# Performance work log

Measured on AMD Instinct MI355X. Metric: run time of the kernel, lower is better.

The kernel has to match this reference:

```python
import jax, jax.numpy as jnp
import numpy as np

DIM = 512
HEADS = 4
HEAD_DIM = DIM // HEADS
SCALE = HEAD_DIM ** -0.5


def _lin(x, W, b):
    # torch nn.Linear: y = x @ W.T + b, W is [out, in]
    return jnp.einsum('...i,oi->...o', x, W) + b


def setup_inputs() -> dict:
    key = jax.random.key(0)
    ks = jax.random.split(key, 20)
    f1 = jax.random.normal(ks[0], (4, 5, DIM, 10, 10), dtype=jnp.float32)
    f2 = jax.random.normal(ks[1], (4, 75, DIM, 10, 10), dtype=jnp.float32)
    names = ['k1', 'v1', 'q2', 'k2', 'v2', 'o1', 'o2']
    inp = {'f1': f1, 'f2': f2}
    for i, nm in enumerate(names):
        inp['W' + nm] = 0.02 * jax.random.normal(ks[2 + 2 * i], (DIM, DIM), dtype=jnp.float32)
        inp['b' + nm] = 0.02 * jax.random.normal(ks[3 + 2 * i], (DIM,), dtype=jnp.float32)
    return inp


def _forward(f1, f2, Wk1, bk1, Wv1, bv1, Wq2, bq2, Wk2, bk2, Wv2, bv2, Wo1, bo1, Wo2, bo2):
    B, n1, C, H, W = f1.shape
    n2 = f2.shape[1]
    L = H * W
    # [B,n,C,H,W] -> [B,n,L,C]
    f1t = f1.reshape(B, n1, C, L).transpose(0, 1, 3, 2)
    f2t = f2.reshape(B, n2, C, L).transpose(0, 1, 3, 2)

    def split_heads(x, n):  # [B,n,L,C] -> [B,heads,n*L,hd]
        return x.reshape(B, n * L, HEADS, HEAD_DIM).transpose(0, 2, 1, 3)

    def merge_heads(x, n):  # [B,heads,n*L,hd] -> [B,n,L,C]
        return x.transpose(0, 2, 1, 3).reshape(B, n, L, C)

    K1 = split_heads(_lin(f1t, Wk1, bk1), n1)
    V1 = split_heads(_lin(f1t, Wv1, bv1), n1)
    Q2 = split_heads(_lin(f2t, Wq2, bq2), n2)
    K2 = split_heads(_lin(f2t, Wk2, bk2), n2)  # computed as in original, unused downstream
    V2 = split_heads(_lin(f2t, Wv2, bv2), n2)

    # Query attends to support: [B,h,n2*L,n1*L]
    att_q = jax.nn.softmax(jnp.einsum('bhqd,bhkd->bhqk', Q2, K1) * SCALE, axis=-1)
    out2 = jnp.einsum('bhqk,bhkd->bhqd', att_q, V1)
    out2 = _lin(merge_heads(out2, n2), Wo2, bo2)
    out2 = out2.transpose(0, 1, 3, 2).reshape(B, n2, C, H, W)

    # Support attends to query: [B,h,n1*L,n2*L]
    att_s = jax.nn.softmax(jnp.einsum('bhsd,bhqd->bhsq', K1, Q2) * SCALE, axis=-1)
    out1 = jnp.einsum('bhsq,bhqd->bhsd', att_s, V2)
    out1 = _lin(merge_heads(out1, n1), Wo1, bo1)
    out1 = out1.transpose(0, 1, 3, 2).reshape(B, n1, C, H, W)
    return (out1, out2)


def reference(f1, f2, Wk1, bk1, Wv1, bv1, Wq2, bq2, Wk2, bk2, Wv2, bv2, Wo1, bo1, Wo2, bo2):
    return _forward(f1, f2, Wk1, bk1, Wv1, bv1, Wq2, bq2, Wk2, bk2, Wv2, bv2, Wo1, bo1, Wo2, bo2)
```

## Files before the change

kernel.cpp:

```cpp
#include <hip/hip_runtime.h>
#include <hip/hip_bf16.h>


#define QSCL  (0.08838834764831845f * 1.4426950408889634f)
#define KSPL  8
#define NRB2  59
#define NRB1  4

using bf16x8 = __attribute__((ext_vector_type(8))) short;
using f32x4  = __attribute__((ext_vector_type(4))) float;

__device__ inline ushort f2bf(float x) {
    union { float f; unsigned u; } v; v.f = x;
    unsigned r = v.u + 0x7fff + ((v.u >> 16) & 1);
    return (ushort)(r >> 16);
}

__device__ inline void gll16(const ushort* g, ushort* l) {
    __builtin_amdgcn_global_load_lds(
        (const __attribute__((address_space(1))) void*)g,
        (__attribute__((address_space(3))) void*)l, 16, 0, 0);
}

struct PreArgs { const float* w[6]; float s[6]; const float* f1; const float* f2; };

__global__ __launch_bounds__(256) void pre_kernel(
    PreArgs pa, ushort* __restrict__ Wb,
    ushort* __restrict__ f1t, ushort* __restrict__ f2t)
{
    __shared__ ushort Ts[100 * 136];
    const int t   = threadIdx.x;
    const int bid = blockIdx.x;

    if (bid < 1536) {
        const int wsel = bid >> 8;
        const float* src = pa.w[wsel];
        const float sc = pa.s[wsel];
        ushort* d = Wb + (size_t)wsel * 262144;
        const int idx = ((bid & 255) * 256 + t) * 4;
        const float4 v = *(const float4*)(src + idx);
        ushort4 o;
        o.x = f2bf(v.x * sc); o.y = f2bf(v.y * sc);
        o.z = f2bf(v.z * sc); o.w = f2bf(v.w * sc);
        *(ushort4*)(d + idx) = o;
        return;
    }

    const int bn = bid - 1536;
    const float* Xb;
    ushort* Yb;
    if (bn < 20) { Xb = pa.f1 + (size_t)bn * 51200;        Yb = f1t + (size_t)bn * 51200; }
    else         { Xb = pa.f2 + (size_t)(bn - 20) * 51200; Yb = f2t + (size_t)(bn - 20) * 51200; }

    for (int c0 = 0; c0 < 512; c0 += 128) {
        __syncthreads();
        #pragma unroll
        for (int i = 0; i < 50; ++i) {
            const int id = i * 256 + t;
            const int c = id / 100, l = id - c * 100;
            Ts[l * 136 + c] = f2bf(Xb[(size_t)(c0 + c) * 100 + l]);
        }
        __syncthreads();
        #pragma unroll
        for (int i = 0; i < 7; ++i) {
            const int id = i * 256 + t;
            if (id < 1600) {
                const int cg = id & 15, l = id >> 4;
                *(uint4*)(Yb + (size_t)l * 512 + c0 + cg * 8) =
                    *(const uint4*)&Ts[l * 136 + cg * 8];
            }
        }
    }
}

struct GemmJob {
    const ushort* A; const ushort* B;
    const float* bias; void* C;
    size_t sA, sB, sC;
    float bscale;
    int ldC, Mrows, Ncols, gx, gy, fastn, baxis, nblk;
};

struct GemmJobs { GemmJob j0, j1, j2, j3; int ntot; };

template<int EPI>
__global__ __launch_bounds__(256) void gemm_nt(GemmJobs J)
{
    __shared__ ushort smem[17408];
    ushort* As = smem;
    ushort* Bs = smem + 8192;

    const int ntot = J.ntot;
    const int q8 = ntot >> 3, r8 = ntot & 7;
    const int xcd = blockIdx.x & 7, ii = blockIdx.x >> 3;
    const int work = (xcd < r8 ? xcd * (q8 + 1)
                               : r8 * (q8 + 1) + (xcd - r8) * q8) + ii;

    GemmJob j; int id;
    {
        const int c0 = J.j0.nblk;
        const int c1 = c0 + J.j1.nblk;
        const int c2 = c1 + J.j2.nblk;
        if (work < c0)      { j = J.j0; id = work; }
        else if (work < c1) { j = J.j1; id = work - c0; }
        else if (work < c2) { j = J.j2; id = work - c1; }
        else                { j = J.j3; id = work - c2; }
    }

    const int fx = id % j.gx;
    const int rem = id / j.gx;
    const int fy = rem % j.gy;
    const int bz = rem / j.gy;
    const int m0 = (j.fastn ? fy : fx) * 128;
    const int n0 = (j.fastn ? fx : fy) * 128;

    const int t    = threadIdx.x;
    const int lane = t & 63;
    const int w    = t >> 6;
    const int mw   = (w >> 1) * 64;
    const int nw   = (w & 1) * 64;
    const int Mrows = j.Mrows, Ncols = j.Ncols, ldC = j.ldC;
    const ushort* Ab = j.A + (size_t)bz * j.sA;
    const ushort* Bb = j.B + (size_t)bz * j.sB;
    const float* bias = j.bias;

    f32x4 acc[4][4];
    #pragma unroll
    for (int i = 0; i < 4; ++i)
        #pragma unroll
        for (int jj = 0; jj < 4; ++jj) acc[i][jj] = (f32x4){0.f, 0.f, 0.f, 0.f};

    const int lr = lane >> 3;
    const int cb = lane & 7;

    for (int k0 = 0; k0 < 512; k0 += 64) {
        if (k0) __syncthreads();
        #pragma unroll
        for (int i = 0; i < 4; ++i) {
            const int row = w * 32 + i * 8 + lr;
            const int ar = min(m0 + row, Mrows - 1);
            gll16(Ab + (size_t)ar * 512 + k0 + ((cb ^ (row & 7)) * 8),
                  As + (w * 32 + i * 8) * 64);
            const int br = min(n0 + row, Ncols - 1);
            gll16(Bb + (size_t)br * 512 + k0 + ((cb ^ (row & 7)) * 8),
                  Bs + (w * 32 + i * 8) * 64);
        }
        __syncthreads();
        #pragma unroll
        for (int ks = 0; ks < 2; ++ks) {
            bf16x8 af[4], bv[4];
            #pragma unroll
            for (int mf = 0; mf < 4; ++mf) {
                const int row = mw + mf * 16 + (lane & 15);
                af[mf] = *(const bf16x8*)((const char*)As + row * 128 +
                          ((ks * 64 + (lane >> 4) * 16) ^ ((row & 7) << 4)));
            }
            #pragma unroll
            for (int nf = 0; nf < 4; ++nf) {
                const int row = nw + nf * 16 + (lane & 15);
                bv[nf] = *(const bf16x8*)((const char*)Bs + row * 128 +
                          ((ks * 64 + (lane >> 4) * 16) ^ ((row & 7) << 4)));
            }
            #pragma unroll
            for (int mf = 0; mf < 4; ++mf)
                #pragma unroll
                for (int nf = 0; nf < 4; ++nf)
                    acc[mf][nf] = __builtin_amdgcn_mfma_f32_16x16x32_bf16(
                        af[mf], bv[nf], acc[mf][nf], 0, 0, 0);
        }
    }
    __syncthreads();

    if (EPI == 0) {
        float bcol[4];
        if (j.baxis == 1) {
            #pragma unroll
            for (int nf = 0; nf < 4; ++nf)
                bcol[nf] = bias[n0 + nw + nf * 16 + (lane & 15)] * j.bscale;
        }
        ushort* Ts = smem;
        #pragma unroll
        for (int mf = 0; mf < 4; ++mf) {
            #pragma unroll
            for (int r = 0; r < 4; ++r) {
                const int row = mw + mf * 16 + (lane >> 4) * 4 + r;
                const float brow = (j.baxis == 0) ? bias[m0 + row] * j.bscale : 0.f;
                #pragma unroll
                for (int nf = 0; nf < 4; ++nf) {
                    const int col = nw + nf * 16 + (lane & 15);
                    const float v = acc[mf][nf][r] +
                                    ((j.baxis == 1) ? bcol[nf] : brow);
                    Ts[row * 136 + col] = f2bf(v);
                }
            }
        }
        __syncthreads();
        ushort* Cb = (ushort*)j.C + (size_t)bz * j.sC;
        #pragma unroll
        for (int i = 0; i < 8; ++i) {
            const int id2 = i * 256 + t;
            const int row = id2 >> 4, cg = id2 & 15;
            if (m0 + row < Mrows)
                *(uint4*)(Cb + (size_t)(m0 + row) * ldC + n0 + cg * 8) =
                    *(const uint4*)&Ts[row * 136 + cg * 8];
        }
    } else {
        float* Ts2 = (float*)smem;
        float* Cb = (float*)j.C + (size_t)bz * j.sC;
        const int colL = t & 127;
        const int rb2 = t >> 7;
        const int tg = n0 + colL;
        int nIdx = 0, lIdx = 0;
        if (tg < Ncols) { nIdx = tg / 100; lIdx = tg - nIdx * 100; }
        #pragma unroll
        for (int h = 0; h < 2; ++h) {
            __syncthreads();
            if ((mw >> 6) == h) {
                #pragma unroll
                for (int mf = 0; mf < 4; ++mf) {
                    #pragma unroll
                    for (int r = 0; r < 4; ++r) {
                        const int rowl = mf * 16 + (lane >> 4) * 4 + r;
                        const float brow = bias[m0 + h * 64 + rowl];
                        #pragma unroll
                        for (int nf = 0; nf < 4; ++nf) {
                            const int col = nw + nf * 16 + (lane & 15);
                            Ts2[rowl * 132 + col] = acc[mf][nf][r] + brow;
                        }
                    }
                }
            }
            __syncthreads();
            if (tg < Ncols) {
                float* dst = Cb + (size_t)nIdx * 51200 + lIdx;
                #pragma unroll
                for (int i = 0; i < 32; ++i) {
                    const int rowl = i * 2 + rb2;
                    const int c = m0 + h * 64 + rowl;
                    dst[(size_t)c * 100] = Ts2[rowl * 132 + colL];
                }
            }
        }
    }
}

__global__ __launch_bounds__(256, 2) void attn_mfma_kernel(
    const ushort* __restrict__ Q2, const ushort* __restrict__ K1,
    const ushort* __restrict__ V1t, const ushort* __restrict__ V2t,
    ushort* __restrict__ A2, float* __restrict__ PartO, float* __restrict__ Pml)
{
    __shared__ ushort Ks[64 * 128];
    __shared__ ushort Vs[128 * 64];

    const int t    = threadIdx.x;
    const int lane = t & 63;
    const int w    = t >> 6;

    const int flat = blockIdx.x;
    const int xcd = flat & 7, ii = flat >> 3;
    const bool dir2 = (ii >= 64);
    int rb, h, b, sp = 0;
    if (dir2) {
        const int w2 = xcd * 118 + (ii - 64);
        rb = w2 % NRB2;
        const int hb = w2 / NRB2;
        h = hb & 3; b = hb >> 2;
    } else {
        const int w1 = xcd * 64 + ii;
        rb = w1 & 3; sp = (w1 >> 2) & 7;
        const int hb = w1 >> 5;
        h = hb & 3; b = hb >> 2;
    }

    const int TR = dir2 ? 7500 : 500;
    const int TK = dir2 ? 500 : 7500;
    const int strideV = dir2 ? 512 : 7552;
    const ushort* R  = dir2 ? Q2 : K1;
    const ushort* Kt = dir2 ? K1 : Q2;
    const ushort* Vt = dir2 ? V1t : V2t;

    const int r0 = rb * 128;
    const int ho = h * 128;

    int kbeg = 0, kend = TK;
    if (!dir2) {
        kbeg = sp * 938;
        kend = kbeg + 938; if (kend > TK) kend = TK;
    }

    bf16x8 qa0[4], qa1[4];
    {
        const ushort* Rb = R + (size_t)b * TR * 512;
        const int q0 = min(r0 + w * 32 + (lane & 15), TR - 1);
        const int q1 = min(r0 + w * 32 + 16 + (lane & 15), TR - 1);
        const ushort* qp0 = Rb + (size_t)q0 * 512 + ho + (lane >> 4) * 8;
        const ushort* qp1 = Rb + (size_t)q1 * 512 + ho + (lane >> 4) * 8;
        #pragma unroll
        for (int s = 0; s < 4; ++s) {
            qa0[s] = *(const bf16x8*)(qp0 + s * 32);
            qa1[s] = *(const bf16x8*)(qp1 + s * 32);
        }
    }

    const ushort* Kb = Kt + (size_t)b * TK * 512;
    const ushort* Vb = Vt + ((size_t)b * 512 + ho) * strideV;

    const int krow_i = lane >> 4;
    const int kcol   = (lane & 15) * 8;
    const int vrow_i = lane >> 3;
    const int vcol   = (lane & 7) * 8;
    const int gq     = lane >> 4;

    float m_run0 = -3.0e38f, l_run0 = 0.f;
    float m_run1 = -3.0e38f, l_run1 = 0.f;
    f32x4 acc0[8], acc1[8];
    #pragma unroll
    for (int g = 0; g < 8; ++g) {
        acc0[g] = (f32x4){0.f, 0.f, 0.f, 0.f};
        acc1[g] = (f32x4){0.f, 0.f, 0.f, 0.f};
    }

    #pragma unroll
    for (int i = 0; i < 4; ++i) {
        const int kr = w * 16 + i * 4 + krow_i;
        gll16(Kb + (size_t)(kbeg + kr) * 512 + ho + (kcol ^ ((kr & 7) << 3)),
              Ks + (w * 16 + i * 4) * 128);
    }

    for (int kbase = kbeg; kbase < kend; kbase += 64) {
        #pragma unroll
        for (int i = 0; i < 4; ++i) {
            const int vd = w * 32 + i * 8 + vrow_i;
            gll16(Vb + (size_t)vd * strideV + kbase + (vcol ^ ((vd & 7) << 3)),
                  Vs + (w * 32 + i * 8) * 64);
        }
        asm volatile("s_waitcnt vmcnt(4)" ::: "memory");
        __builtin_amdgcn_s_barrier();
        __builtin_amdgcn_sched_barrier(0);

        f32x4 sf0[4], sf1[4];
        __builtin_amdgcn_s_setprio(1);
        #pragma unroll
        for (int f = 0; f < 4; ++f) {
            f32x4 s0 = (f32x4){0.f, 0.f, 0.f, 0.f};
            f32x4 s1 = (f32x4){0.f, 0.f, 0.f, 0.f};
            const int kr = f * 16 + (lane & 15);
            const int kb2 = kr * 256, sw = (kr & 7) << 4, g16 = gq * 16;
            #pragma unroll
            for (int s4 = 0; s4 < 4; ++s4) {
                bf16x8 kf = *(const bf16x8*)((const char*)Ks + kb2 + ((s4 * 64 + g16) ^ sw));
                s0 = __builtin_amdgcn_mfma_f32_16x16x32_bf16(kf, qa0[s4], s0, 0, 0, 0);
                s1 = __builtin_amdgcn_mfma_f32_16x16x32_bf16(kf, qa1[s4], s1, 0, 0, 0);
            }
            sf0[f] = s0; sf1[f] = s1;
        }
        __builtin_amdgcn_s_setprio(0);

        if (kbase + 64 > kend) {
            #pragma unroll
            for (int f = 0; f < 4; ++f)
                #pragma unroll
                for (int r = 0; r < 4; ++r)
                    if (kbase + f * 16 + gq * 4 + r >= kend) {
                        sf0[f][r] = -3.0e38f; sf1[f][r] = -3.0e38f;
                    }
        }
        {
            float mx = sf0[0][0];
            #pragma unroll
            for (int f = 0; f < 4; ++f)
                #pragma unroll
                for (int r = 0; r < 4; ++r) mx = fmaxf(mx, sf0[f][r]);
            mx = fmaxf(mx, __shfl_xor(mx, 16));
            mx = fmaxf(mx, __shfl_xor(mx, 32));
            if (__any(mx > m_run0 + 11.0f)) {
                const float mn = fmaxf(m_run0, mx);
                const float sc = __builtin_amdgcn_exp2f(m_run0 - mn);
                m_run0 = mn; l_run0 *= sc;
                float scal4[4];
                #pragma unroll
                for (int r = 0; r < 4; ++r)
                    scal4[r] = __shfl(sc, (lane & 48) + gq * 4 + r);
                #pragma unroll
                for (int g = 0; g < 8; ++g)
                    #pragma unroll
                    for (int r = 0; r < 4; ++r) acc0[g][r] *= scal4[r];
            }
            float rs = 0.f;
            #pragma unroll
            for (int f = 0; f < 4; ++f)
                #pragma unroll
                for (int r = 0; r < 4; ++r) {
                    const float p = __builtin_amdgcn_exp2f(sf0[f][r] - m_run0);
                    sf0[f][r] = p; rs += p;
                }
            rs += __shfl_xor(rs, 16);
            rs += __shfl_xor(rs, 32);
            l_run0 += rs;
        }
        {
            float mx = sf1[0][0];
            #pragma unroll
            for (int f = 0; f < 4; ++f)
                #pragma unroll
                for (int r = 0; r < 4; ++r) mx = fmaxf(mx, sf1[f][r]);
            mx = fmaxf(mx, __shfl_xor(mx, 16));
            mx = fmaxf(mx, __shfl_xor(mx, 32));
            if (__any(mx > m_run1 + 11.0f)) {
                const float mn = fmaxf(m_run1, mx);
                const float sc = __builtin_amdgcn_exp2f(m_run1 - mn);
                m_run1 = mn; l_run1 *= sc;
                float scal4[4];
                #pragma unroll
                for (int r = 0; r < 4; ++r)
                    scal4[r] = __shfl(sc, (lane & 48) + gq * 4 + r);
                #pragma unroll
                for (int g = 0; g < 8; ++g)
                    #pragma unroll
                    for (int r = 0; r < 4; ++r) acc1[g][r] *= scal4[r];
            }
            float rs = 0.f;
            #pragma unroll
            for (int f = 0; f < 4; ++f)
                #pragma unroll
                for (int r = 0; r < 4; ++r) {
                    const float p = __builtin_amdgcn_exp2f(sf1[f][r] - m_run1);
                    sf1[f][r] = p; rs += p;
                }
            rs += __shfl_xor(rs, 16);
            rs += __shfl_xor(rs, 32);
            l_run1 += rs;
        }

        union { uint u[4]; bf16x8 v; } pa00, pa01, pa10, pa11;
        {
            uint pk0[4][2], pk1[4][2];
            #pragma unroll
            for (int f = 0; f < 4; ++f) {
                asm("v_cvt_pk_bf16_f32 %0, %1, %2" : "=v"(pk0[f][0]) : "v"(sf0[f][0]), "v"(sf0[f][1]));
                asm("v_cvt_pk_bf16_f32 %0, %1, %2" : "=v"(pk0[f][1]) : "v"(sf0[f][2]), "v"(sf0[f][3]));
                asm("v_cvt_pk_bf16_f32 %0, %1, %2" : "=v"(pk1[f][0]) : "v"(sf1[f][0]), "v"(sf1[f][1]));
                asm("v_cvt_pk_bf16_f32 %0, %1, %2" : "=v"(pk1[f][1]) : "v"(sf1[f][2]), "v"(sf1[f][3]));
            }
            #pragma unroll
            for (int u = 0; u < 4; ++u) {
                const int srcl = (lane & 15) + ((lane & 16) << 1) + ((u >> 1) << 4);
                const uint a0 = (uint)__shfl((int)pk0[0][u & 1], srcl);
                const uint b0 = (uint)__shfl((int)pk0[1][u & 1], srcl);
                const uint a1 = (uint)__shfl((int)pk0[2][u & 1], srcl);
                const uint b1 = (uint)__shfl((int)pk0[3][u & 1], srcl);
                pa00.u[u] = (lane & 32) ? b0 : a0;
                pa01.u[u] = (lane & 32) ? b1 : a1;
                const uint c0 = (uint)__shfl((int)pk1[0][u & 1], srcl);
                const uint d0 = (uint)__shfl((int)pk1[1][u & 1], srcl);
                const uint c1 = (uint)__shfl((int)pk1[2][u & 1], srcl);
                const uint d1 = (uint)__shfl((int)pk1[3][u & 1], srcl);
                pa10.u[u] = (lane & 32) ? d0 : c0;
                pa11.u[u] = (lane & 32) ? d1 : c1;
            }
        }

        asm volatile("s_waitcnt vmcnt(0)" ::: "memory");
        __builtin_amdgcn_s_barrier();
        __builtin_amdgcn_sched_barrier(0);

        if (kbase + 64 < kend) {
            #pragma unroll
            for (int i = 0; i < 4; ++i) {
                const int kr = w * 16 + i * 4 + krow_i;
                gll16(Kb + (size_t)(kbase + 64 + kr) * 512 + ho + (kcol ^ ((kr & 7) << 3)),
                      Ks + (w * 16 + i * 4) * 128);
            }
        }

        {
            const int g16 = gq * 16;
            __builtin_amdgcn_s_setprio(1);
            #pragma unroll
            for (int g = 0; g < 8; ++g) {
                const int dr = g * 16 + (lane & 15);
                const int vb = dr * 128, vsw = (dr & 7) << 4;
                bf16x8 v0 = *(const bf16x8*)((const char*)Vs + vb + ((g16) ^ vsw));
                bf16x8 v1 = *(const bf16x8*)((const char*)Vs + vb + ((64 + g16) ^ vsw));
                acc0[g] = __builtin_amdgcn_mfma_f32_16x16x32_bf16(pa00.v, v0, acc0[g], 0, 0, 0);
                acc0[g] = __builtin_amdgcn_mfma_f32_16x16x32_bf16(pa01.v, v1, acc0[g], 0, 0, 0);
                acc1[g] = __builtin_amdgcn_mfma_f32_16x16x32_bf16(pa10.v, v0, acc1[g], 0, 0, 0);
                acc1[g] = __builtin_amdgcn_mfma_f32_16x16x32_bf16(pa11.v, v1, acc1[g], 0, 0, 0);
            }
            __builtin_amdgcn_s_setprio(0);
        }
        __builtin_amdgcn_s_barrier();
        __builtin_amdgcn_sched_barrier(0);
    }

    if (dir2) {
        float linv0[4], linv1[4];
        #pragma unroll
        for (int r = 0; r < 4; ++r) {
            linv0[r] = 1.f / __shfl(l_run0, (lane & 48) + gq * 4 + r);
            linv1[r] = 1.f / __shfl(l_run1, (lane & 48) + gq * 4 + r);
        }
        #pragma unroll
        for (int r = 0; r < 4; ++r) {
            const int row0 = r0 + w * 32 + (gq << 2) + r;
            if (row0 < TR) {
                ushort* Ab2 = A2 + ((size_t)b * TR + row0) * 512 + ho + (lane & 15);
                #pragma unroll
                for (int g = 0; g < 8; ++g) Ab2[g * 16] = f2bf(acc0[g][r] * linv0[r]);
            }
            const int row1 = r0 + w * 32 + 16 + (gq << 2) + r;
            if (row1 < TR) {
                ushort* Ab2 = A2 + ((size_t)b * TR + row1) * 512 + ho + (lane & 15);
                #pragma unroll
                for (int g = 0; g < 8; ++g) Ab2[g * 16] = f2bf(acc1[g][r] * linv1[r]);
            }
        }
    } else {
        const size_t tile = (((size_t)b * 4 + h) * NRB1 + rb) * KSPL + sp;
        float* Po = PartO + tile * (128 * 128);
        float* Pm = Pml + tile * 256;
        #pragma unroll
        for (int r = 0; r < 4; ++r) {
            const int row0 = w * 32 + (gq << 2) + r;
            float* pp0 = Po + row0 * 128 + (lane & 15);
            #pragma unroll
            for (int g = 0; g < 8; ++g) pp0[g * 16] = acc0[g][r];
            const int row1 = w * 32 + 16 + (gq << 2) + r;
            float* pp1 = Po + row1 * 128 + (lane & 15);
            #pragma unroll
            for (int g = 0; g < 8; ++g) pp1[g * 16] = acc1[g][r];
        }
        if (lane < 16) {
            Pm[w * 32 + lane] = m_run0;
            Pm[w * 32 + 16 + lane] = m_run1;
            Pm[128 + w * 32 + lane] = l_run0;
            Pm[128 + w * 32 + 16 + lane] = l_run1;
        }
    }
}

__global__ __launch_bounds__(256) void attn_combine_kernel(
    const float* __restrict__ PartO, const float* __restrict__ Pml,
    ushort* __restrict__ Aout, int TR)
{
    const int t = threadIdx.x;
    const int rb = blockIdx.x >> 1, half = blockIdx.x & 1;
    const int h = blockIdx.y, b = blockIdx.z;
    const int row = half * 64 + (t >> 2);
    const int dq = (t & 3) * 32;
    const int r0 = rb * 128;
    const size_t tbase = (((size_t)b * 4 + h) * NRB1 + rb) * KSPL;

    float M = -3.0e38f;
    #pragma unroll
    for (int i = 0; i < KSPL; ++i)
        M = fmaxf(M, Pml[(tbase + i) * 256 + row]);
    float wt[KSPL], L = 0.f;
    #pragma unroll
    for (int i = 0; i < KSPL; ++i) {
        const float wi = __builtin_amdgcn_exp2f(Pml[(tbase + i) * 256 + row] - M);
        wt[i] = wi;
        L += wi * Pml[(tbase + i) * 256 + 128 + row];
    }
    if (r0 + row >= TR) return;
    const float invL = 1.f / L;

    float o[32];
    #pragma unroll
    for (int j = 0; j < 32; ++j) o[j] = 0.f;
    #pragma unroll
    for (int i = 0; i < KSPL; ++i) {
        const float* pp = PartO + (tbase + i) * (128 * 128) + row * 128 + dq;
        #pragma unroll
        for (int j = 0; j < 32; j += 4) {
            const float4 v = *(const float4*)(pp + j);
            o[j] += wt[i] * v.x; o[j+1] += wt[i] * v.y;
            o[j+2] += wt[i] * v.z; o[j+3] += wt[i] * v.w;
        }
    }
    ushort* Ab = Aout + ((size_t)b * TR + r0 + row) * 512 + h * 128 + dq;
    #pragma unroll
    for (int j = 0; j < 32; j += 4) {
        ushort4 v;
        v.x = f2bf(o[j] * invL); v.y = f2bf(o[j+1] * invL);
        v.z = f2bf(o[j+2] * invL); v.w = f2bf(o[j+3] * invL);
        *(ushort4*)(Ab + j) = v;
    }
}

extern "C" void kernel_launch(void* const* d_in, const int* in_sizes, int n_in,
                              void* d_out, int out_size, void* d_ws, size_t ws_size,
                              hipStream_t stream) {
    const float* f1  = (const float*)d_in[0];
    const float* f2  = (const float*)d_in[1];
    const float* Wk1 = (const float*)d_in[2];
    const float* bk1 = (const float*)d_in[3];
    const float* Wv1 = (const float*)d_in[4];
    const float* bv1 = (const float*)d_in[5];
    const float* Wq2 = (const float*)d_in[6];
    const float* bq2 = (const float*)d_in[7];
    const float* Wv2 = (const float*)d_in[10];
    const float* bv2 = (const float*)d_in[11];
    const float* Wo1 = (const float*)d_in[12];
    const float* bo1 = (const float*)d_in[13];
    const float* Wo2 = (const float*)d_in[14];
    const float* bo2 = (const float*)d_in[15];
    float* out = (float*)d_out;

    ushort* f1t = (ushort*)d_ws;
    ushort* f2t = f1t + (size_t)1024000;
    ushort* Wb  = f2t + (size_t)15360000;
    ushort* K1  = Wb  + (size_t)1572864;
    ushort* Q2  = K1  + (size_t)1024000;
    ushort* V1t = Q2  + (size_t)15360000;
    ushort* V2t = V1t + (size_t)1048576;
    ushort* A1  = V2t + (size_t)15466496;
    ushort* A2  = A1  + (size_t)1024000;
    float* PartO = (float*)(A2 + (size_t)15360000);
    float* Pml   = PartO + (size_t)512*128*128;

    const dim3 blk(256);

    const ushort* Wk1b = Wb;
    const ushort* Wv1b = Wb + 262144;
    const ushort* Wq2b = Wb + 2*262144;
    const ushort* Wv2b = Wb + 3*262144;
    const ushort* Wo1b = Wb + 4*262144;
    const ushort* Wo2b = Wb + 5*262144;

    PreArgs pa;
    pa.w[0]=Wk1; pa.w[1]=Wv1; pa.w[2]=Wq2; pa.w[3]=Wv2; pa.w[4]=Wo1; pa.w[5]=Wo2;
    pa.s[0]=1.f; pa.s[1]=1.f; pa.s[2]=QSCL; pa.s[3]=1.f; pa.s[4]=1.f; pa.s[5]=1.f;
    pa.f1 = f1; pa.f2 = f2;
    pre_kernel<<<dim3(1856), blk, 0, stream>>>(pa, Wb, f1t, f2t);

    GemmJob jK {f1t, Wk1b, bk1, K1, 0, 0, 0, 1.f, 512, 2000, 512,
                4, 16, 1, 1, 64};
    GemmJob jQ {f2t, Wq2b, bq2, Q2, 0, 0, 0, QSCL, 512, 30000, 512,
                4, 235, 1, 1, 940};
    GemmJob jV1{Wv1b, f1t, bv1, V1t, 0, (size_t)500*512, (size_t)512*512, 1.f,
                512, 512, 500, 4, 4, 0, 0, 64};
    GemmJob jV2{Wv2b, f2t, bv2, V2t, 0, (size_t)7500*512, (size_t)512*7552, 1.f,
                7552, 512, 7500, 4, 59, 0, 0, 944};
    GemmJobs JP{jK, jQ, jV1, jV2, 2012};
    gemm_nt<0><<<dim3(2012), blk, 0, stream>>>(JP);

    attn_mfma_kernel<<<dim3(1456), dim3(256), 0, stream>>>(
        Q2, K1, V1t, V2t, A2, PartO, Pml);
    attn_combine_kernel<<<dim3(8, 4, 4), blk, 0, stream>>>(PartO, Pml, A1, 500);

    GemmJob jO1{Wo1b, A1, bo1, out, 0, (size_t)500*512, (size_t)5*51200, 1.f,
                0, 512, 500, 4, 4, 0, 0, 64};
    GemmJob jO2{Wo2b, A2, bo2, out + (size_t)1024000, 0, (size_t)7500*512,
                (size_t)75*51200, 1.f, 0, 512, 7500, 4, 59, 0, 0, 944};
    GemmJob jZ{};
    GemmJobs JO{jO1, jO2, jZ, jZ, 1008};
    gemm_nt<2><<<dim3(1008), blk, 0, stream>>>(JO);
}
```

Measured before the change: 233.8 us.

## Double-buffer K and V tiles in LDS for attention loop

Splits the K and V shared-memory tiles into two buffers so the next tile's K and V global-to-LDS loads are issued at the start of each iteration and overlap with both the QK and PV MFMA phases. This replaces the earlier scheme, where V was loaded and waited on inside the iteration and K was prefetched only before PV. LDS use per block doubles to 64KB, which may limit how many blocks fit per CU under launch_bounds(256,2). It also drops one barrier per iteration.

```diff
diff --git a/kernel.cpp b/kernel.cpp
--- a/kernel.cpp
+++ b/kernel.cpp
@@ -249,8 +249,8 @@
     const ushort* __restrict__ V1t, const ushort* __restrict__ V2t,
     ushort* __restrict__ A2, float* __restrict__ PartO, float* __restrict__ Pml)
 {
-    __shared__ ushort Ks[64 * 128];
-    __shared__ ushort Vs[128 * 64];
+    __shared__ ushort Ks[2 * 64 * 128];
+    __shared__ ushort Vs[2 * 128 * 64];
 
     const int t    = threadIdx.x;
     const int lane = t & 63;
@@ -325,18 +325,33 @@
         const int kr = w * 16 + i * 4 + krow_i;
         gll16(Kb + (size_t)(kbeg + kr) * 512 + ho + (kcol ^ ((kr & 7) << 3)),
               Ks + (w * 16 + i * 4) * 128);
-    }
-
-    for (int kbase = kbeg; kbase < kend; kbase += 64) {
-        #pragma unroll
-        for (int i = 0; i < 4; ++i) {
-            const int vd = w * 32 + i * 8 + vrow_i;
-            gll16(Vb + (size_t)vd * strideV + kbase + (vcol ^ ((vd & 7) << 3)),
-                  Vs + (w * 32 + i * 8) * 64);
-        }
-        asm volatile("s_waitcnt vmcnt(4)" ::: "memory");
-        __builtin_amdgcn_s_barrier();
-        __builtin_amdgcn_sched_barrier(0);
+        const int vd = w * 32 + i * 8 + vrow_i;
+        gll16(Vb + (size_t)vd * strideV + kbeg + (vcol ^ ((vd & 7) << 3)),
+              Vs + (w * 32 + i * 8) * 64);
+    }
+    asm volatile("s_waitcnt vmcnt(0)" ::: "memory");
+    __builtin_amdgcn_s_barrier();
+    __builtin_amdgcn_sched_barrier(0);
+
+    int c = 0;
+    for (int kbase = kbeg; kbase < kend; kbase += 64, ++c) {
+        const ushort* KsC = Ks + (c & 1) * 8192;
+        const ushort* VsC = Vs + (c & 1) * 8192;
+        ushort* KsN = Ks + ((c + 1) & 1) * 8192;
+        ushort* VsN = Vs + ((c + 1) & 1) * 8192;
+
+        const int kn = kbase + 64;
+        if (kn < kend) {
+            #pragma unroll
+            for (int i = 0; i < 4; ++i) {
+                const int kr = w * 16 + i * 4 + krow_i;
+                gll16(Kb + (size_t)(kn + kr) * 512 + ho + (kcol ^ ((kr & 7) << 3)),
+                      KsN + (w * 16 + i * 4) * 128);
+                const int vd = w * 32 + i * 8 + vrow_i;
+                gll16(Vb + (size_t)vd * strideV + kn + (vcol ^ ((vd & 7) << 3)),
+                      VsN + (w * 32 + i * 8) * 64);
+            }
+        }
 
         f32x4 sf0[4], sf1[4];
         __builtin_amdgcn_s_setprio(1);
@@ -348,7 +363,7 @@
             const int kb2 = kr * 256, sw = (kr & 7) << 4, g16 = gq * 16;
             #pragma unroll
             for (int s4 = 0; s4 < 4; ++s4) {
-                bf16x8 kf = *(const bf16x8*)((const char*)Ks + kb2 + ((s4 * 64 + g16) ^ sw));
+                bf16x8 kf = *(const bf16x8*)((const char*)KsC + kb2 + ((s4 * 64 + g16) ^ sw));
                 s0 = __builtin_amdgcn_mfma_f32_16x16x32_bf16(kf, qa0[s4], s0, 0, 0, 0);
                 s1 = __builtin_amdgcn_mfma_f32_16x16x32_bf16(kf, qa1[s4], s1, 0, 0, 0);
             }
@@ -460,19 +475,6 @@
             }
         }
 
-        asm volatile("s_waitcnt vmcnt(0)" ::: "memory");
-        __builtin_amdgcn_s_barrier();
-        __builtin_amdgcn_sched_barrier(0);
-
-        if (kbase + 64 < kend) {
-            #pragma unroll
-            for (int i = 0; i < 4; ++i) {
-                const int kr = w * 16 + i * 4 + krow_i;
-                gll16(Kb + (size_t)(kbase + 64 + kr) * 512 + ho + (kcol ^ ((kr & 7) << 3)),
-                      Ks + (w * 16 + i * 4) * 128);
-            }
-        }
-
         {
             const int g16 = gq * 16;
             __builtin_amdgcn_s_setprio(1);
@@ -480,8 +482,8 @@
             for (int g = 0; g < 8; ++g) {
                 const int dr = g * 16 + (lane & 15);
                 const int vb = dr * 128, vsw = (dr & 7) << 4;
-                bf16x8 v0 = *(const bf16x8*)((const char*)Vs + vb + ((g16) ^ vsw));
-                bf16x8 v1 = *(const bf16x8*)((const char*)Vs + vb + ((64 + g16) ^ vsw));
+                bf16x8 v0 = *(const bf16x8*)((const char*)VsC + vb + ((g16) ^ vsw));
+                bf16x8 v1 = *(const bf16x8*)((const char*)VsC + vb + ((64 + g16) ^ vsw));
                 acc0[g] = __builtin_amdgcn_mfma_f32_16x16x32_bf16(pa00.v, v0, acc0[g], 0, 0, 0);
                 acc0[g] = __builtin_amdgcn_mfma_f32_16x16x32_bf16(pa01.v, v1, acc0[g], 0, 0, 0);
                 acc1[g] = __builtin_amdgcn_mfma_f32_16x16x32_bf16(pa10.v, v0, acc1[g], 0, 0, 0);
@@ -489,6 +491,8 @@
             }
             __builtin_amdgcn_s_setprio(0);
         }
+
+        asm volatile("s_waitcnt vmcnt(0)" ::: "memory");
         __builtin_amdgcn_s_barrier();
         __builtin_amdgcn_sched_barrier(0);
     }
```

Result: no change. 232.3 us, median of 2 (-0.6%).
